# Kernel optimization log

Hardware: AMD Instinct MI355X
Metric: run time of the kernel (lower is better)

Reference implementation:

```python
import jax, jax.numpy as jnp
import numpy as np

BATCH = 262144

def _f64_bits_msb_first(val):
    # IEEE754 double bit pattern, MSB first (equivalent to struct.pack('>d', val))
    u = int(np.frombuffer(np.float64(val).tobytes(), dtype=np.uint64)[0])
    return [float((u >> (63 - i)) & 1) for i in range(64)]

def setup_inputs() -> dict:
    key = jax.random.key(0)
    # Table T[j] = bits of 2^(j/64), shape [64 entries, 64 bits]
    table = np.array([_f64_bits_msb_first(2.0 ** (j / 64.0)) for j in range(64)],
                     dtype=np.float32)
    idx_bits = jax.random.randint(key, (BATCH, 6), 0, 2).astype(jnp.int32)
    return {"table_bits": jnp.asarray(table), "idx_bits": idx_bits}

def reference(table_bits, idx_bits):
    """Fused MUX-tree table lookup.

    Each MUXGate(sel, B, A) = sel ? B : A on binary pulses. Level k selects on
    idx_bits[..., k] (MSB first) between the lower and upper half of the
    surviving table entries, exactly reproducing the 6-level tree of 64-bit MUXes.
    """
    batch_shape = idx_bits.shape[:-1]
    # [B, 64 entries, 64 bits]
    x = jnp.broadcast_to(table_bits, batch_shape + table_bits.shape)
    for k in range(6):  # b5 (weight 32) down to b0 (weight 1)
        n = x.shape[-2] // 2
        sel = (idx_bits[..., k] > 0)[..., None, None]
        x = jnp.where(sel, x[..., n:, :], x[..., :n, :])
    return x[..., 0, :]  # [B, 64] bit pulses of 2^(idx/64)
```

## Files before the change

kernel.cpp:

```cpp
#include <hip/hip_runtime.h>


#define ROWS 256

typedef float nfloat4 __attribute__((ext_vector_type(4)));
#define GLOBAL_AS __attribute__((address_space(1)))
#define LDS_AS    __attribute__((address_space(3)))

__global__ __launch_bounds__(256) void
spike_lut_kernel(const float* __restrict__ table,
                 const int* __restrict__ idx_bits,
                 nfloat4* __restrict__ out4,
                 int batch) {
    __shared__ nfloat4 s_table[64 * 16];
    __shared__ int     s_raw[ROWS * 6];
    __shared__ int     s_idx[ROWS];

    const int  tid  = threadIdx.x;
    const int  wv   = tid >> 6;
    const int  ln   = tid & 63;
    const long b0   = (long)blockIdx.x * ROWS;
    const bool full = (b0 + ROWS) <= batch;

    const nfloat4* t4  = (const nfloat4*)table;
    const int*     src = idx_bits + b0 * 6;

    if (full) {
        #pragma unroll
        for (int r = 0; r < 4; ++r) {
            const int e = r * 256 + wv * 64;
            __builtin_amdgcn_global_load_lds(
                (const GLOBAL_AS void*)(t4 + e + ln),
                (LDS_AS void*)&s_table[e], 16, 0, 0);
        }
        #pragma unroll
        for (int r = 0; r < 6; ++r) {
            const int e = r * 256 + wv * 64;
            __builtin_amdgcn_global_load_lds(
                (const GLOBAL_AS void*)(src + e + ln),
                (LDS_AS void*)&s_raw[e], 4, 0, 0);
        }
    } else {
        #pragma unroll
        for (int r = 0; r < 4; ++r)
            s_table[r * 256 + tid] = t4[r * 256 + tid];
        const long lim = ((long)batch - b0) * 6;
        #pragma unroll
        for (int r = 0; r < 6; ++r) {
            const int g = r * 256 + tid;
            s_raw[g] = (g < lim) ? src[g] : 0;
        }
    }
    __syncthreads();

    {
        const int* p = &s_raw[tid * 6];
        int idx = 0;
        #pragma unroll
        for (int k = 0; k < 6; ++k)
            idx = (idx << 1) | (p[k] > 0 ? 1 : 0);
        s_idx[tid] = idx;
    }
    __syncthreads();

    if (full) {
        #pragma unroll
        for (int it = 0; it < 16; ++it) {
            const int g  = it * 256 + tid;
            const int bl = g >> 4;
            const int q  = g & 15;
            out4[(b0 + bl) * 16 + q] = s_table[s_idx[bl] * 16 + q];
        }
    } else {
        #pragma unroll
        for (int it = 0; it < 16; ++it) {
            const int g  = it * 256 + tid;
            const int bl = g >> 4;
            const int q  = g & 15;
            if (b0 + bl < batch)
                out4[(b0 + bl) * 16 + q] = s_table[s_idx[bl] * 16 + q];
        }
    }
}

extern "C" void kernel_launch(void* const* d_in, const int* in_sizes, int n_in,
                              void* d_out, int out_size, void* d_ws, size_t ws_size,
                              hipStream_t stream) {
    const float* table    = (const float*)d_in[0];
    const int*   idx_bits = (const int*)d_in[1];
    nfloat4*     out4     = (nfloat4*)d_out;

    const int batch  = in_sizes[1] / 6;
    const int blocks = (batch + ROWS - 1) / ROWS;

    spike_lut_kernel<<<blocks, 256, 0, stream>>>(table, idx_bits, out4, batch);
}
```

Measured before the change: 80.35 us.

## Compute row indices in registers and broadcast via wave shuffles

Each thread now loads its own row's six index ints directly as three int2 vector loads and builds the 6-bit index in a register. The LDS staging buffers and the second barrier go away, and per-row indices reach the output lanes through __shfl within the wavefront. Block size doubles to 512 threads and rows, so the table is staged into LDS half as many times. Each thread's index reads are now strided rather than fully coalesced, and larger blocks may reduce scheduling flexibility.

```diff
diff --git a/kernel.cpp b/kernel.cpp
--- a/kernel.cpp
+++ b/kernel.cpp
@@ -1,84 +1,65 @@
 #include <hip/hip_runtime.h>
 
 
-#define ROWS 256
+#define THREADS 512
+#define ROWS    512
 
 typedef float nfloat4 __attribute__((ext_vector_type(4)));
+typedef int   nint2   __attribute__((ext_vector_type(2)));
 #define GLOBAL_AS __attribute__((address_space(1)))
 #define LDS_AS    __attribute__((address_space(3)))
 
-__global__ __launch_bounds__(256) void
+__global__ __launch_bounds__(THREADS) void
 spike_lut_kernel(const float* __restrict__ table,
                  const int* __restrict__ idx_bits,
                  nfloat4* __restrict__ out4,
                  int batch) {
     __shared__ nfloat4 s_table[64 * 16];
-    __shared__ int     s_raw[ROWS * 6];
-    __shared__ int     s_idx[ROWS];
 
-    const int  tid  = threadIdx.x;
-    const int  wv   = tid >> 6;
-    const int  ln   = tid & 63;
-    const long b0   = (long)blockIdx.x * ROWS;
-    const bool full = (b0 + ROWS) <= batch;
+    const int  tid = threadIdx.x;
+    const int  wv  = tid >> 6;
+    const int  ln  = tid & 63;
+    const long b0  = (long)blockIdx.x * ROWS;
 
-    const nfloat4* t4  = (const nfloat4*)table;
-    const int*     src = idx_bits + b0 * 6;
+    const nfloat4* t4 = (const nfloat4*)table;
 
-    if (full) {
-        #pragma unroll
-        for (int r = 0; r < 4; ++r) {
-            const int e = r * 256 + wv * 64;
-            __builtin_amdgcn_global_load_lds(
-                (const GLOBAL_AS void*)(t4 + e + ln),
-                (LDS_AS void*)&s_table[e], 16, 0, 0);
-        }
-        #pragma unroll
-        for (int r = 0; r < 6; ++r) {
-            const int e = r * 256 + wv * 64;
-            __builtin_amdgcn_global_load_lds(
-                (const GLOBAL_AS void*)(src + e + ln),
-                (LDS_AS void*)&s_raw[e], 4, 0, 0);
-        }
-    } else {
-        #pragma unroll
-        for (int r = 0; r < 4; ++r)
-            s_table[r * 256 + tid] = t4[r * 256 + tid];
-        const long lim = ((long)batch - b0) * 6;
-        #pragma unroll
-        for (int r = 0; r < 6; ++r) {
-            const int g = r * 256 + tid;
-            s_raw[g] = (g < lim) ? src[g] : 0;
-        }
+    #pragma unroll
+    for (int r = 0; r < 2; ++r) {
+        const int e = r * 512 + wv * 64;
+        __builtin_amdgcn_global_load_lds(
+            (const GLOBAL_AS void*)(t4 + e + ln),
+            (LDS_AS void*)&s_table[e], 16, 0, 0);
     }
+
+    const long row  = b0 + tid;
+    int        myidx = 0;
+    if (row < batch) {
+        const nint2* p = (const nint2*)(idx_bits + row * 6);
+        const nint2 a = p[0], b = p[1], c = p[2];
+        myidx = ((a.x > 0) << 5) | ((a.y > 0) << 4) |
+                ((b.x > 0) << 3) | ((b.y > 0) << 2) |
+                ((c.x > 0) << 1) |  (c.y > 0);
+    }
+
     __syncthreads();
 
-    {
-        const int* p = &s_raw[tid * 6];
-        int idx = 0;
-        #pragma unroll
-        for (int k = 0; k < 6; ++k)
-            idx = (idx << 1) | (p[k] > 0 ? 1 : 0);
-        s_idx[tid] = idx;
-    }
-    __syncthreads();
-
-    if (full) {
+    const int q = ln & 15;
+    if (b0 + ROWS <= batch) {
         #pragma unroll
         for (int it = 0; it < 16; ++it) {
-            const int g  = it * 256 + tid;
-            const int bl = g >> 4;
-            const int q  = g & 15;
-            out4[(b0 + bl) * 16 + q] = s_table[s_idx[bl] * 16 + q];
+            const int  s    = it * 4 + (ln >> 4);
+            const int  ridx = __shfl(myidx, s, 64);
+            const long r    = b0 + wv * 64 + s;
+            out4[r * 16 + q] = s_table[ridx * 16 + q];
         }
     } else {
         #pragma unroll
         for (int it = 0; it < 16; ++it) {
-            const int g  = it * 256 + tid;
-            const int bl = g >> 4;
-            const int q  = g & 15;
-            if (b0 + bl < batch)
-                out4[(b0 + bl) * 16 + q] = s_table[s_idx[bl] * 16 + q];
+            const int  s    = it * 4 + (ln >> 4);
+            const int  ridx = __shfl(myidx, s, 64);
+            const long r    = b0 + wv * 64 + s;
+            if (r < batch)
+                out4[r * 16 + q] = s_table[ridx * 16 + q];
         }
     }
 }
@@ -93,5 +74,5 @@
     const int batch  = in_sizes[1] / 6;
     const int blocks = (batch + ROWS - 1) / ROWS;
 
-    spike_lut_kernel<<<blocks, 256, 0, stream>>>(table, idx_bits, out4, batch);
+    spike_lut_kernel<<<blocks, THREADS, 0, stream>>>(table, idx_bits, out4, batch);
 }
```

Result: no change. 80.10 us (-0.3%).
